# Kernel tuning notes

Hardware: AMD Instinct MI355X
Metric: run time of the kernel (lower is better)

The kernel has to match this reference:

```python
import jax, jax.numpy as jnp
import numpy as np

EPS = 1e-5
NUM_GROUPS = 8


def setup_inputs() -> dict:
    key = jax.random.key(0)
    ks = jax.random.split(key, 7)
    B, C, D, H, W = 2, 128, 16, 16, 16
    s = 1.0 / np.sqrt(C)
    return {
        "x": jax.random.normal(ks[0], (B, C, D, H, W), dtype=jnp.float32),
        "Wq": jax.random.normal(ks[1], (C, C), dtype=jnp.float32) * s,
        "Wk": jax.random.normal(ks[2], (C, C), dtype=jnp.float32) * s,
        "Wv": jax.random.normal(ks[3], (C, C), dtype=jnp.float32) * s,
        "Wo": jax.random.normal(ks[4], (C, C), dtype=jnp.float32) * s,
        "gamma": jnp.ones((C,), dtype=jnp.float32),
        "beta": jnp.zeros((C,), dtype=jnp.float32),
    }


def reference(x, Wq, Wk, Wv, Wo, gamma, beta):
    B, C = x.shape[0], x.shape[1]
    spatial = x.shape[2:]
    xf = x.reshape(B, C, -1)  # [B, C, N]

    # 1x1 conv == channel-mixing matmul
    q = jnp.einsum('oc,bcn->bon', Wq, xf)
    k = jnp.einsum('oc,bcn->bon', Wk, xf)
    v = jnp.einsum('oc,bcn->bon', Wv, xf)

    # unscaled attention: qk[b,n,m] = sum_c q[b,c,n] k[b,c,m]
    w = jax.nn.softmax(jnp.einsum('bcn,bcm->bnm', q, k), axis=-1)  # [B, N, N]
    # h = v @ w^T : h[b,c,n] = sum_m v[b,c,m] w[b,n,m]
    h = jnp.einsum('bcm,bnm->bcn', v, w)
    h = jnp.einsum('oc,bcn->bon', Wo, h)

    y = xf + h
    # GroupNorm(8, C) over (C//G, N) per group
    g = y.reshape(B, NUM_GROUPS, C // NUM_GROUPS, -1)
    mu = jnp.mean(g, axis=(2, 3), keepdims=True)
    var = jnp.mean(jnp.square(g - mu), axis=(2, 3), keepdims=True)
    gn = ((g - mu) * jax.lax.rsqrt(var + EPS)).reshape(B, C, -1)
    out = gn * gamma[None, :, None] + beta[None, :, None]
    out = out * jax.nn.sigmoid(out)  # SiLU
    return out.reshape(B, C, *spatial)
```

## Files before the change

kernel.cpp:

```cpp
#include <hip/hip_runtime.h>

#define CC 128
#define NN 4096
#define NB 2
#define NSPLIT 4
#define TK 64
#define ITERS 16

typedef unsigned short ushort;
typedef unsigned int uint;
typedef __attribute__((ext_vector_type(8))) _Float16 h8;
typedef __attribute__((ext_vector_type(8))) short s8;
typedef __attribute__((ext_vector_type(4))) float f4;
#define MFMA16(a, b, c) __builtin_amdgcn_mfma_f32_16x16x32_f16(a, b, c, 0, 0, 0)
#define MFMAB(a, b, c)  __builtin_amdgcn_mfma_f32_16x16x32_bf16(a, b, c, 0, 0, 0)

__device__ __forceinline__ ushort f2h(float f) {
  _Float16 h = (_Float16)f;
  return *(ushort*)&h;
}
__device__ __forceinline__ ushort f2bf(float f) {
  uint u = __float_as_uint(f);
  u += 0x7fffu + ((u >> 16) & 1u);
  return (ushort)(u >> 16);
}
__device__ __forceinline__ float bf2f(ushort u) {
  return __uint_as_float((uint)u << 16);
}

__global__ __launch_bounds__(256) void qkv_mm(
    const float* __restrict__ x, const float* __restrict__ Wq,
    const float* __restrict__ Wk, const float* __restrict__ Wv,
    ushort* __restrict__ qT, ushort* __restrict__ kT, ushort* __restrict__ vB,
    float* __restrict__ stats) {
  __shared__ ushort Wh[3][CC][136];
  __shared__ ushort xs[32][136];
  const int t = threadIdx.x;
  const int n0 = blockIdx.x * 32;
  const int b = blockIdx.y;

  if (blockIdx.x == 0 && b == 0 && t < 32) stats[t] = 0.f;

  {
    int c0 = (t & 31) * 4;
    int n4 = (t >> 5) * 4;
    float4 r0 = *(const float4*)&x[((size_t)b * CC + c0 + 0) * NN + n0 + n4];
    float4 r1 = *(const float4*)&x[((size_t)b * CC + c0 + 1) * NN + n0 + n4];
    float4 r2 = *(const float4*)&x[((size_t)b * CC + c0 + 2) * NN + n0 + n4];
    float4 r3 = *(const float4*)&x[((size_t)b * CC + c0 + 3) * NN + n0 + n4];
    ushort4 w0, w1, w2, w3;
    w0.x = f2h(r0.x); w0.y = f2h(r1.x); w0.z = f2h(r2.x); w0.w = f2h(r3.x);
    w1.x = f2h(r0.y); w1.y = f2h(r1.y); w1.z = f2h(r2.y); w1.w = f2h(r3.y);
    w2.x = f2h(r0.z); w2.y = f2h(r1.z); w2.z = f2h(r2.z); w2.w = f2h(r3.z);
    w3.x = f2h(r0.w); w3.y = f2h(r1.w); w3.z = f2h(r2.w); w3.w = f2h(r3.w);
    *(ushort4*)&xs[n4 + 0][c0] = w0;
    *(ushort4*)&xs[n4 + 1][c0] = w1;
    *(ushort4*)&xs[n4 + 2][c0] = w2;
    *(ushort4*)&xs[n4 + 3][c0] = w3;
  }

#pragma unroll
  for (int which = 0; which < 3; ++which) {
    const float* W = (which == 0) ? Wq : (which == 1) ? Wk : Wv;
#pragma unroll
    for (int i = 0; i < 16; ++i) {
      int slot = t + 256 * i;
      int o = slot >> 5, c4 = (slot & 31) * 4;
      float4 w4 = *(const float4*)&W[o * CC + c4];
      ushort4 p; p.x = f2h(w4.x); p.y = f2h(w4.y); p.z = f2h(w4.z); p.w = f2h(w4.w);
      *(ushort4*)&Wh[which][o][c4] = p;
    }
  }
  __syncthreads();

  const int wv = t >> 6, lane = t & 63;
  const int quad = lane >> 4, l16 = lane & 15;

#pragma unroll
  for (int which = 0; which < 2; ++which) {
    ushort* out = which ? kT : qT;
    f4 acc[2][2];
#pragma unroll
    for (int ot = 0; ot < 2; ++ot)
#pragma unroll
      for (int nt = 0; nt < 2; ++nt) acc[ot][nt] = (f4){0.f, 0.f, 0.f, 0.f};
#pragma unroll
    for (int kk = 0; kk < 4; ++kk) {
      h8 a0 = *(const h8*)&Wh[which][(wv * 2 + 0) * 16 + l16][kk * 32 + quad * 8];
      h8 a1 = *(const h8*)&Wh[which][(wv * 2 + 1) * 16 + l16][kk * 32 + quad * 8];
#pragma unroll
      for (int nt = 0; nt < 2; ++nt) {
        h8 bb = *(const h8*)&xs[nt * 16 + l16][kk * 32 + quad * 8];
        acc[0][nt] = MFMA16(a0, bb, acc[0][nt]);
        acc[1][nt] = MFMA16(a1, bb, acc[1][nt]);
      }
    }
#pragma unroll
    for (int ot = 0; ot < 2; ++ot)
#pragma unroll
      for (int nt = 0; nt < 2; ++nt) {
        f4 a = acc[ot][nt];
        ushort4 p; p.x = f2h(a[0]); p.y = f2h(a[1]); p.z = f2h(a[2]); p.w = f2h(a[3]);
        *(ushort4*)&out[((size_t)b * NN + n0 + nt * 16 + l16) * CC +
                        (wv * 2 + ot) * 16 + quad * 4] = p;
      }
  }

  {
    f4 acc[2][2];
#pragma unroll
    for (int ci = 0; ci < 2; ++ci)
#pragma unroll
      for (int nt = 0; nt < 2; ++nt) acc[ci][nt] = (f4){0.f, 0.f, 0.f, 0.f};
#pragma unroll
    for (int kk = 0; kk < 4; ++kk) {
      h8 a0 = *(const h8*)&xs[0 * 16 + l16][kk * 32 + quad * 8];
      h8 a1 = *(const h8*)&xs[1 * 16 + l16][kk * 32 + quad * 8];
      h8 b0 = *(const h8*)&Wh[2][(wv * 2 + 0) * 16 + l16][kk * 32 + quad * 8];
      h8 b1 = *(const h8*)&Wh[2][(wv * 2 + 1) * 16 + l16][kk * 32 + quad * 8];
      acc[0][0] = MFMA16(a0, b0, acc[0][0]);
      acc[0][1] = MFMA16(a1, b0, acc[0][1]);
      acc[1][0] = MFMA16(a0, b1, acc[1][0]);
      acc[1][1] = MFMA16(a1, b1, acc[1][1]);
    }
#pragma unroll
    for (int ci = 0; ci < 2; ++ci)
#pragma unroll
      for (int nt = 0; nt < 2; ++nt) {
        f4 a = acc[ci][nt];
        ushort4 p; p.x = f2bf(a[0]); p.y = f2bf(a[1]); p.z = f2bf(a[2]); p.w = f2bf(a[3]);
        *(ushort4*)&vB[((size_t)b * CC + (wv * 2 + ci) * 16 + l16) * NN +
                       n0 + nt * 16 + quad * 4] = p;
      }
  }
}

__global__ __launch_bounds__(256) void attn_split(
    const ushort* __restrict__ qTg, const ushort* __restrict__ kTg,
    const ushort* __restrict__ vBg, ushort* __restrict__ Op,
    float* __restrict__ Lg) {
  __shared__ ushort ksT[TK][136];
  __shared__ ushort vs[CC][72];
  __shared__ ushort psb[4][32][72];

  const int t = threadIdx.x;
  const int b = blockIdx.z;
  const int split = blockIdx.y;
  const int n0 = blockIdx.x * 128;
  const int wv = t >> 6;
  const int lane = t & 63;
  const int quad = lane >> 4;
  const int l16 = lane & 15;
  const int nw = n0 + wv * 32;
  const int m00 = split * (NN / NSPLIT);

  const int krow = t >> 4, kcol = (t & 15) * 8;
  const int vrow = t >> 3, vcol = (t & 7) * 8;
  const ushort* kbp = kTg + ((size_t)b * NN + m00 + krow) * CC + kcol;
  const ushort* vbp = vBg + ((size_t)b * CC + vrow) * NN + m00 + vcol;

  const size_t qb0 = ((size_t)b * NN + nw + l16) * CC + quad * 8;
  const size_t qb1 = qb0 + (size_t)16 * CC;
  h8 aq[2][4];
#pragma unroll
  for (int kk = 0; kk < 4; ++kk) {
    aq[0][kk] = *(const h8*)&qTg[qb0 + kk * 32];
    aq[1][kk] = *(const h8*)&qTg[qb1 + kk * 32];
  }

  int4 k0 = *(const int4*)&kbp[0];
  int4 k1 = *(const int4*)&kbp[16 * CC];
  int4 k2 = *(const int4*)&kbp[32 * CC];
  int4 k3 = *(const int4*)&kbp[48 * CC];
  int4 v0 = *(const int4*)&vbp[0];
  int4 v1 = *(const int4*)&vbp[(size_t)32 * NN];
  int4 v2 = *(const int4*)&vbp[(size_t)64 * NN];
  int4 v3 = *(const int4*)&vbp[(size_t)96 * NN];

  s8 ones;
#pragma unroll
  for (int i = 0; i < 8; ++i) ones[i] = (short)0x3F80;

  f4 o[2][8];
#pragma unroll
  for (int j = 0; j < 2; ++j)
#pragma unroll
    for (int ct = 0; ct < 8; ++ct) o[j][ct] = (f4){0.f, 0.f, 0.f, 0.f};
  f4 oL[2];
  oL[0] = (f4){0.f, 0.f, 0.f, 0.f};
  oL[1] = (f4){0.f, 0.f, 0.f, 0.f};

  for (int kt = 0; kt < ITERS; ++kt) {
    *(int4*)&ksT[krow][kcol]      = k0;
    *(int4*)&ksT[krow + 16][kcol] = k1;
    *(int4*)&ksT[krow + 32][kcol] = k2;
    *(int4*)&ksT[krow + 48][kcol] = k3;
    *(int4*)&vs[vrow][vcol]       = v0;
    *(int4*)&vs[vrow + 32][vcol]  = v1;
    *(int4*)&vs[vrow + 64][vcol]  = v2;
    *(int4*)&vs[vrow + 96][vcol]  = v3;
    __syncthreads();

    {
      int ktn = (kt + 1 < ITERS) ? kt + 1 : kt;
      const ushort* kp = kbp + (size_t)ktn * TK * CC;
      const ushort* vp = vbp + (size_t)ktn * TK;
      k0 = *(const int4*)&kp[0];
      k1 = *(const int4*)&kp[16 * CC];
      k2 = *(const int4*)&kp[32 * CC];
      k3 = *(const int4*)&kp[48 * CC];
      v0 = *(const int4*)&vp[0];
      v1 = *(const int4*)&vp[(size_t)32 * NN];
      v2 = *(const int4*)&vp[(size_t)64 * NN];
      v3 = *(const int4*)&vp[(size_t)96 * NN];
    }

    f4 s[2][4];
#pragma unroll
    for (int j = 0; j < 2; ++j)
#pragma unroll
      for (int mt = 0; mt < 4; ++mt) s[j][mt] = (f4){0.f, 0.f, 0.f, 0.f};
#pragma unroll
    for (int kk = 0; kk < 4; ++kk) {
      h8 b0 = *(const h8*)&ksT[ 0 + l16][kk * 32 + quad * 8];
      h8 b1 = *(const h8*)&ksT[16 + l16][kk * 32 + quad * 8];
      h8 b2 = *(const h8*)&ksT[32 + l16][kk * 32 + quad * 8];
      h8 b3 = *(const h8*)&ksT[48 + l16][kk * 32 + quad * 8];
#pragma unroll
      for (int j = 0; j < 2; ++j) {
        s[j][0] = MFMA16(b0, aq[j][kk], s[j][0]);
        s[j][1] = MFMA16(b1, aq[j][kk], s[j][1]);
        s[j][2] = MFMA16(b2, aq[j][kk], s[j][2]);
        s[j][3] = MFMA16(b3, aq[j][kk], s[j][3]);
      }
    }

#pragma unroll
    for (int j = 0; j < 2; ++j)
#pragma unroll
      for (int mt = 0; mt < 4; ++mt) {
        ushort4 pk;
        pk.x = f2bf(__expf(s[j][mt][0]));
        pk.y = f2bf(__expf(s[j][mt][1]));
        pk.z = f2bf(__expf(s[j][mt][2]));
        pk.w = f2bf(__expf(s[j][mt][3]));
        *(ushort4*)&psb[wv][j * 16 + l16][mt * 16 + quad * 4] = pk;
      }

#pragma unroll
    for (int mk = 0; mk < 2; ++mk) {
      s8 bp0 = *(const s8*)&psb[wv][ 0 + l16][mk * 32 + quad * 8];
      s8 bp1 = *(const s8*)&psb[wv][16 + l16][mk * 32 + quad * 8];
#pragma unroll
      for (int ct = 0; ct < 8; ++ct) {
        s8 a = *(const s8*)&vs[ct * 16 + l16][mk * 32 + quad * 8];
        o[0][ct] = MFMAB(a, bp0, o[0][ct]);
        o[1][ct] = MFMAB(a, bp1, o[1][ct]);
      }
      oL[0] = MFMAB(ones, bp0, oL[0]);
      oL[1] = MFMAB(ones, bp1, oL[1]);
    }
    __syncthreads();
  }

#pragma unroll
  for (int j = 0; j < 2; ++j) {
    if (quad == 0)
      Lg[((size_t)(split * NB + b)) * NN + nw + j * 16 + l16] = oL[j][0];
    size_t nb_ = ((size_t)(split * NB + b) * NN + nw + j * 16 + l16) * CC + quad * 4;
    ushort4 p;
#pragma unroll
    for (int ct = 0; ct < 8; ++ct) {
      f4 a = o[j][ct];
      p.x = f2bf(a[0]); p.y = f2bf(a[1]); p.z = f2bf(a[2]); p.w = f2bf(a[3]);
      *(ushort4*)&Op[nb_ + ct * 16] = p;
    }
  }
}

__global__ __launch_bounds__(256) void proj_mm(
    const float* __restrict__ x, const float* __restrict__ Wo,
    const ushort* __restrict__ Op, const float* __restrict__ Lg,
    float* __restrict__ y, float* __restrict__ stats) {
  __shared__ ushort Wh[CC][136];
  __shared__ ushort hT[32][136];
  __shared__ float Linv[32];
  const int t = threadIdx.x;
  const int n0 = blockIdx.x * 32;
  const int b = blockIdx.y;

#pragma unroll
  for (int i = 0; i < 16; ++i) {
    int slot = t + 256 * i;
    int o = slot >> 5, c4 = (slot & 31) * 4;
    float4 w4 = *(const float4*)&Wo[o * CC + c4];
    ushort4 p; p.x = f2h(w4.x); p.y = f2h(w4.y); p.z = f2h(w4.z); p.w = f2h(w4.w);
    *(ushort4*)&Wh[o][c4] = p;
  }
  if (t < 32) {
    float l = 0.f;
#pragma unroll
    for (int s = 0; s < NSPLIT; ++s)
      l += Lg[(size_t)(s * NB + b) * NN + n0 + t];
    Linv[t] = 1.f / l;
  }
  __syncthreads();

#pragma unroll
  for (int i = 0; i < 16; ++i) {
    int slot = t + 256 * i;
    int n = slot >> 5, c4 = (slot & 31) * 4;
    size_t base = ((size_t)(n0 + n)) * CC + c4;
    float a0 = 0.f, a1 = 0.f, a2 = 0.f, a3 = 0.f;
#pragma unroll
    for (int s = 0; s < NSPLIT; ++s) {
      ushort4 u = *(const ushort4*)&Op[(size_t)(s * NB + b) * NN * CC + base];
      a0 += bf2f(u.x); a1 += bf2f(u.y); a2 += bf2f(u.z); a3 += bf2f(u.w);
    }
    float li = Linv[n];
    ushort4 p;
    p.x = f2h(a0 * li); p.y = f2h(a1 * li);
    p.z = f2h(a2 * li); p.w = f2h(a3 * li);
    *(ushort4*)&hT[n][c4] = p;
  }
  __syncthreads();

  const int wv = t >> 6, lane = t & 63;
  const int quad = lane >> 4, l16 = lane & 15;

  f4 acc[2][2];
#pragma unroll
  for (int nt = 0; nt < 2; ++nt)
#pragma unroll
    for (int ot = 0; ot < 2; ++ot) acc[nt][ot] = (f4){0.f, 0.f, 0.f, 0.f};
#pragma unroll
  for (int kk = 0; kk < 4; ++kk) {
    h8 a0 = *(const h8*)&hT[0 * 16 + l16][kk * 32 + quad * 8];
    h8 a1 = *(const h8*)&hT[1 * 16 + l16][kk * 32 + quad * 8];
    h8 b0 = *(const h8*)&Wh[(wv * 2 + 0) * 16 + l16][kk * 32 + quad * 8];
    h8 b1 = *(const h8*)&Wh[(wv * 2 + 1) * 16 + l16][kk * 32 + quad * 8];
    acc[0][0] = MFMA16(a0, b0, acc[0][0]);
    acc[0][1] = MFMA16(a0, b1, acc[0][1]);
    acc[1][0] = MFMA16(a1, b0, acc[1][0]);
    acc[1][1] = MFMA16(a1, b1, acc[1][1]);
  }

#pragma unroll
  for (int ot = 0; ot < 2; ++ot) {
    const int o = (wv * 2 + ot) * 16 + l16;
    const int g = wv * 2 + ot;
    float s = 0.f, sq = 0.f;
#pragma unroll
    for (int nt = 0; nt < 2; ++nt) {
      size_t addr = ((size_t)b * CC + o) * NN + n0 + nt * 16 + quad * 4;
      float4 xv = *(const float4*)&x[addr];
      f4 a = acc[nt][ot];
      float4 yy;
      yy.x = a[0] + xv.x; yy.y = a[1] + xv.y;
      yy.z = a[2] + xv.z; yy.w = a[3] + xv.w;
      *(float4*)&y[addr] = yy;
      s += yy.x + yy.y + yy.z + yy.w;
      sq += yy.x * yy.x + yy.y * yy.y + yy.z * yy.z + yy.w * yy.w;
    }
#pragma unroll
    for (int off = 1; off < 64; off <<= 1) {
      s += __shfl_xor(s, off);
      sq += __shfl_xor(sq, off);
    }
    if (lane == 0) {
      atomicAdd(&stats[(b * 8 + g) * 2 + 0], s);
      atomicAdd(&stats[(b * 8 + g) * 2 + 1], sq);
    }
  }
}

__global__ __launch_bounds__(256) void gn_silu(
    const float* __restrict__ y, const float* __restrict__ stats,
    const float* __restrict__ gamma, const float* __restrict__ beta,
    float* __restrict__ out) {
  const int tid = blockIdx.x * 256 + threadIdx.x;
  const int i4 = tid * 4;
  const int c = (i4 >> 12) & (CC - 1);
  const int b = i4 >> 19;
  const int g = c >> 4;
  const float inv = 1.f / 65536.f;
  float sum = stats[(b * 8 + g) * 2 + 0];
  float sq  = stats[(b * 8 + g) * 2 + 1];
  float mean = sum * inv;
  float var = sq * inv - mean * mean;
  float rs = rsqrtf(var + 1e-5f);
  float ga = gamma[c], be = beta[c];
  float4 v4 = *(const float4*)&y[i4];
  float4 r;
  float o;
  o = (v4.x - mean) * rs * ga + be; r.x = o / (1.f + __expf(-o));
  o = (v4.y - mean) * rs * ga + be; r.y = o / (1.f + __expf(-o));
  o = (v4.z - mean) * rs * ga + be; r.z = o / (1.f + __expf(-o));
  o = (v4.w - mean) * rs * ga + be; r.w = o / (1.f + __expf(-o));
  *(float4*)&out[i4] = r;
}

extern "C" void kernel_launch(void* const* d_in, const int* in_sizes, int n_in,
                              void* d_out, int out_size, void* d_ws, size_t ws_size,
                              hipStream_t stream) {
  const float* x     = (const float*)d_in[0];
  const float* Wq    = (const float*)d_in[1];
  const float* Wk    = (const float*)d_in[2];
  const float* Wv    = (const float*)d_in[3];
  const float* Wo    = (const float*)d_in[4];
  const float* gamma = (const float*)d_in[5];
  const float* beta  = (const float*)d_in[6];
  float* out = (float*)d_out;
  float* ws  = (float*)d_ws;

  const size_t M = (size_t)NB * CC * NN;
  ushort* Op = (ushort*)ws;
  ushort* qT = (ushort*)(ws + 2 * M);
  ushort* kT = qT + M;
  float* y = ws + 2 * M;
  ushort* vB = kT + M;
  float* Lg = (float*)(vB + M);
  float* stats = Lg + (size_t)NSPLIT * NB * NN;

  qkv_mm<<<dim3(NN / 32, NB), 256, 0, stream>>>(x, Wq, Wk, Wv, qT, kT, vB, stats);
  attn_split<<<dim3(NN / 128, NSPLIT, NB), 256, 0, stream>>>(qT, kT, vB, Op, Lg);
  proj_mm<<<dim3(NN / 32, NB), 256, 0, stream>>>(x, Wo, Op, Lg, y, stats);
  gn_silu<<<dim3((int)(M / 1024)), 256, 0, stream>>>(y, stats, gamma, beta, out);
}
```

Before: 146.2 us.

## Load K and V fragments directly from global memory, dropping LDS staging

Measured after the change: 187.0 us. 27.9% more time.

```diff
diff --git a/kernel.cpp b/kernel.cpp
--- a/kernel.cpp
+++ b/kernel.cpp
@@ -139,8 +139,6 @@
     const ushort* __restrict__ qTg, const ushort* __restrict__ kTg,
     const ushort* __restrict__ vBg, ushort* __restrict__ Op,
     float* __restrict__ Lg) {
-  __shared__ ushort ksT[TK][136];
-  __shared__ ushort vs[CC][72];
   __shared__ ushort psb[4][32][72];
 
   const int t = threadIdx.x;
@@ -154,11 +152,6 @@
   const int nw = n0 + wv * 32;
   const int m00 = split * (NN / NSPLIT);
 
-  const int krow = t >> 4, kcol = (t & 15) * 8;
-  const int vrow = t >> 3, vcol = (t & 7) * 8;
-  const ushort* kbp = kTg + ((size_t)b * NN + m00 + krow) * CC + kcol;
-  const ushort* vbp = vBg + ((size_t)b * CC + vrow) * NN + m00 + vcol;
-
   const size_t qb0 = ((size_t)b * NN + nw + l16) * CC + quad * 8;
   const size_t qb1 = qb0 + (size_t)16 * CC;
   h8 aq[2][4];
@@ -168,14 +161,8 @@
     aq[1][kk] = *(const h8*)&qTg[qb1 + kk * 32];
   }
 
-  int4 k0 = *(const int4*)&kbp[0];
-  int4 k1 = *(const int4*)&kbp[16 * CC];
-  int4 k2 = *(const int4*)&kbp[32 * CC];
-  int4 k3 = *(const int4*)&kbp[48 * CC];
-  int4 v0 = *(const int4*)&vbp[0];
-  int4 v1 = *(const int4*)&vbp[(size_t)32 * NN];
-  int4 v2 = *(const int4*)&vbp[(size_t)64 * NN];
-  int4 v3 = *(const int4*)&vbp[(size_t)96 * NN];
+  const ushort* kfb = kTg + ((size_t)b * NN + m00 + l16) * CC + quad * 8;
+  const ushort* vfb = vBg + ((size_t)b * CC + l16) * NN + m00 + quad * 8;
 
   s8 ones;
 #pragma unroll
@@ -191,29 +178,8 @@
   oL[1] = (f4){0.f, 0.f, 0.f, 0.f};
 
   for (int kt = 0; kt < ITERS; ++kt) {
-    *(int4*)&ksT[krow][kcol]      = k0;
-    *(int4*)&ksT[krow + 16][kcol] = k1;
-    *(int4*)&ksT[krow + 32][kcol] = k2;
-    *(int4*)&ksT[krow + 48][kcol] = k3;
-    *(int4*)&vs[vrow][vcol]       = v0;
-    *(int4*)&vs[vrow + 32][vcol]  = v1;
-    *(int4*)&vs[vrow + 64][vcol]  = v2;
-    *(int4*)&vs[vrow + 96][vcol]  = v3;
-    __syncthreads();
-
-    {
-      int ktn = (kt + 1 < ITERS) ? kt + 1 : kt;
-      const ushort* kp = kbp + (size_t)ktn * TK * CC;
-      const ushort* vp = vbp + (size_t)ktn * TK;
-      k0 = *(const int4*)&kp[0];
-      k1 = *(const int4*)&kp[16 * CC];
-      k2 = *(const int4*)&kp[32 * CC];
-      k3 = *(const int4*)&kp[48 * CC];
-      v0 = *(const int4*)&vp[0];
-      v1 = *(const int4*)&vp[(size_t)32 * NN];
-      v2 = *(const int4*)&vp[(size_t)64 * NN];
-      v3 = *(const int4*)&vp[(size_t)96 * NN];
-    }
+    const ushort* kp = kfb + (size_t)kt * TK * CC;
+    const ushort* vp = vfb + (size_t)kt * TK;
 
     f4 s[2][4];
 #pragma unroll
@@ -222,10 +188,10 @@
       for (int mt = 0; mt < 4; ++mt) s[j][mt] = (f4){0.f, 0.f, 0.f, 0.f};
 #pragma unroll
     for (int kk = 0; kk < 4; ++kk) {
-      h8 b0 = *(const h8*)&ksT[ 0 + l16][kk * 32 + quad * 8];
-      h8 b1 = *(const h8*)&ksT[16 + l16][kk * 32 + quad * 8];
-      h8 b2 = *(const h8*)&ksT[32 + l16][kk * 32 + quad * 8];
-      h8 b3 = *(const h8*)&ksT[48 + l16][kk * 32 + quad * 8];
+      h8 b0 = *(const h8*)&kp[ 0 * CC + kk * 32];
+      h8 b1 = *(const h8*)&kp[16 * CC + kk * 32];
+      h8 b2 = *(const h8*)&kp[32 * CC + kk * 32];
+      h8 b3 = *(const h8*)&kp[48 * CC + kk * 32];
 #pragma unroll
       for (int j = 0; j < 2; ++j) {
         s[j][0] = MFMA16(b0, aq[j][kk], s[j][0]);
@@ -234,6 +200,13 @@
         s[j][3] = MFMA16(b3, aq[j][kk], s[j][3]);
       }
     }
+
+    s8 va[2][8];
+#pragma unroll
+    for (int mk = 0; mk < 2; ++mk)
+#pragma unroll
+      for (int ct = 0; ct < 8; ++ct)
+        va[mk][ct] = *(const s8*)&vp[(size_t)ct * 16 * NN + mk * 32];
 
 #pragma unroll
     for (int j = 0; j < 2; ++j)
@@ -253,14 +226,12 @@
       s8 bp1 = *(const s8*)&psb[wv][16 + l16][mk * 32 + quad * 8];
 #pragma unroll
       for (int ct = 0; ct < 8; ++ct) {
-        s8 a = *(const s8*)&vs[ct * 16 + l16][mk * 32 + quad * 8];
-        o[0][ct] = MFMAB(a, bp0, o[0][ct]);
-        o[1][ct] = MFMAB(a, bp1, o[1][ct]);
+        o[0][ct] = MFMAB(va[mk][ct], bp0, o[0][ct]);
+        o[1][ct] = MFMAB(va[mk][ct], bp1, o[1][ct]);
       }
       oL[0] = MFMAB(ones, bp0, oL[0]);
       oL[1] = MFMAB(ones, bp1, oL[1]);
     }
-    __syncthreads();
   }
 
 #pragma unroll
```
